# Kernel tuning notes

Measured on AMD Instinct MI355X. Metric: run time of the kernel, lower is better.

## Reference

```python
import jax, jax.numpy as jnp
import numpy as np
import math

B, S, E, H = 4, 1024, 1024, 16
D = E // H
C = 1.0           # Poincare ball curvature
CS = math.sqrt(C)
EPS = 1e-7

def _sq(x):
    return jnp.sum(x * x, axis=-1, keepdims=True)

def expmap0(v):
    n = jnp.sqrt(jnp.clip(_sq(v), 1e-15))
    return jnp.tanh(CS * n) * v / (CS * n)

def logmap0(y):
    n = jnp.sqrt(jnp.clip(_sq(y), 1e-15))
    t = jnp.clip(CS * n, 0.0, 1.0 - 1e-6)
    return jnp.arctanh(t) * y / (CS * n)

def hlinear(x, z, r):
    # Poincare fully-connected layer (HNN++, Shimizu et al.), as in hypll HLinear
    lam = 2.0 / jnp.clip(1.0 - C * _sq(x), EPS)          # [..., 1] conformal factor
    zn = jnp.clip(jnp.linalg.norm(z, axis=0), 1e-15)     # [out]
    xz = x @ z                                           # [..., out]
    tcr = 2.0 * CS * r
    v = (2.0 * zn / CS) * jnp.arcsinh(CS * lam * xz / zn * jnp.cosh(tcr) - (lam - 1.0) * jnp.sinh(tcr))
    w = jnp.sinh(CS * v) / CS
    return w / (1.0 + jnp.sqrt(1.0 + C * jnp.sum(w * w, -1, keepdims=True)))

def _beta(a, b):
    return math.exp(math.lgamma(a) + math.lgamma(b) - math.lgamma(a + b))

def _forward(query, key, value, zq, bq, zk, bk, zv, bv):
    pq, pk, pv = hlinear(query, zq, bq), hlinear(key, zk, bk), hlinear(value, zv, bv)
    split = lambda x: x.reshape(B, S, H, D).transpose(0, 2, 1, 3)   # [B,H,S,D]
    q, k, v = split(pq), split(pk), split(pv)
    # attention_similarity: negative per-head pairwise Poincare distance (all heads vectorized)
    q2 = jnp.sum(q * q, -1)                              # [B,H,Sq]
    k2 = jnp.sum(k * k, -1)                              # [B,H,Sk]
    qk = jnp.einsum('bhqd,bhkd->bhqk', q, k)
    diff2 = jnp.clip(q2[..., :, None] + k2[..., None, :] - 2.0 * qk, 0.0)
    den = jnp.clip((1.0 - C * q2)[..., :, None] * (1.0 - C * k2)[..., None, :], EPS)
    dist = jnp.arccosh(jnp.clip(1.0 + 2.0 * C * diff2 / den, 1.0 + 1e-6)) / CS
    # attention_activation: softmax over keys
    w = jax.nn.softmax(-dist, axis=-1)                   # [B,H,Sq,Sk]
    # attention_midpoint: weighted gyromidpoint of values over keys
    lam = 2.0 / jnp.clip(1.0 - C * jnp.sum(v * v, -1), EPS)          # [B,H,Sk]
    num = jnp.einsum('bhqk,bhkd->bhqd', w * lam[..., None, :], v)
    dnm = jnp.clip(jnp.einsum('bhqk,bhk->bhq', jnp.abs(w), lam - 1.0), EPS)
    u = num / dnm[..., None]
    mid = u / (1.0 + jnp.sqrt(jnp.clip(1.0 - C * _sq(u), EPS)))      # (1/2) Mobius scalar mult
    # manifold.cat: beta-concatenation of heads (HNN++)
    scale = _beta(E / 2.0, 0.5) / _beta(D / 2.0, 0.5)
    tv = logmap0(mid) * scale                            # tangent at origin, [B,H,S,D]
    return expmap0(tv.transpose(0, 2, 1, 3).reshape(B, S, E))

def setup_inputs():
    key = jax.random.key(0)
    ks = jax.random.split(key, 9)
    mk = lambda k: expmap0(jax.random.normal(k, (B, S, E), jnp.float32) * (0.3 / math.sqrt(E)))
    zs = lambda k: jax.random.normal(k, (E, E), jnp.float32) / math.sqrt(E)
    bs = lambda k: jax.random.normal(k, (E,), jnp.float32) * 0.01
    return {"query": mk(ks[0]), "key": mk(ks[1]), "value": mk(ks[2]),
            "zq": zs(ks[3]), "bq": bs(ks[4]), "zk": zs(ks[5]), "bk": bs(ks[6]),
            "zv": zs(ks[7]), "bv": bs(ks[8])}

def reference(query, key, value, zq, bq, zk, bk, zv, bv):
    return _forward(query, key, value, zq, bq, zk, bk, zv, bv)
```

## Files before the change

kernel.cpp:

```cpp
#include <hip/hip_runtime.h>
#include <cmath>

#define EPSF 1e-7f

constexpr int B_ = 4, S_ = 1024, E_ = 1024, H_ = 16, D_ = 64;
constexpr int BS_ = B_ * S_;

typedef __attribute__((ext_vector_type(8))) short bf16x8;
typedef __attribute__((ext_vector_type(4))) float f32x4;

__device__ inline unsigned int fbits(float f) { union { float f; unsigned int u; } x; x.f = f; return x.u; }
__device__ inline float ubits(unsigned int u) { union { unsigned int u; float f; } x; x.u = u; return x.f; }

__device__ inline unsigned short f2bf(float f) {
  unsigned int u = fbits(f);
  unsigned int r = u + 0x7fffu + ((u >> 16) & 1u);
  return (unsigned short)(r >> 16);
}
__device__ inline float bf2f(unsigned short h) { return ubits(((unsigned int)h) << 16); }
__device__ inline float fastrcp(float x) { return __builtin_amdgcn_rcpf(x); }

__device__ __forceinline__ void async_ld16(const unsigned short* g, unsigned short* l) {
  __builtin_amdgcn_global_load_lds(
      (const __attribute__((address_space(1))) unsigned int*)g,
      (__attribute__((address_space(3))) unsigned int*)l, 16, 0, 0);
}

__device__ __forceinline__ unsigned int cvt_pk_bf16(float lo, float hi) {
  unsigned int r;
  asm("v_cvt_pk_bf16_f32 %0, %1, %2" : "=v"(r) : "v"(lo), "v"(hi));
  return r;
}
__device__ __forceinline__ void permlane32_swap(unsigned int &a, unsigned int &b) {
  asm("v_permlane32_swap_b32 %0, %1" : "+v"(a), "+v"(b));
}
__device__ __forceinline__ void permlane16_swap(unsigned int &a, unsigned int &b) {
  asm("v_permlane16_swap_b32 %0, %1" : "+v"(a), "+v"(b));
}

__global__ __launch_bounds__(256) void xsplit_kernel(
    const float* __restrict__ xq, const float* __restrict__ xk,
    const float* __restrict__ xv, unsigned short* __restrict__ Xbf,
    float* __restrict__ lamRow) {
  const int row = blockIdx.x;
  const float* x = (row < BS_) ? xq : (row < 2 * BS_ ? xk : xv);
  const int r = row & (BS_ - 1);
  const int tid = threadIdx.x;
  float4 v = ((const float4*)(x + (size_t)r * E_))[tid];
  float s = v.x * v.x + v.y * v.y + v.z * v.z + v.w * v.w;
  #pragma unroll
  for (int m = 1; m < 64; m <<= 1) s += __shfl_xor(s, m, 64);
  __shared__ float red[4];
  if ((tid & 63) == 0) red[tid >> 6] = s;
  __syncthreads();
  s = red[0] + red[1] + red[2] + red[3];
  uint2 p;
  p.x = (unsigned int)f2bf(v.x) | ((unsigned int)f2bf(v.y) << 16);
  p.y = (unsigned int)f2bf(v.z) | ((unsigned int)f2bf(v.w) << 16);
  ((uint2*)(Xbf + (size_t)row * E_))[tid] = p;
  if (tid == 0) lamRow[row] = 2.0f / fmaxf(1.0f - s, EPSF);
}

__global__ __launch_bounds__(256) void zsplit_kernel(
    const float* __restrict__ zq, const float* __restrict__ zk, const float* __restrict__ zv,
    unsigned short* __restrict__ BhiT, float* __restrict__ Zpart) {
  const int mat = blockIdx.z;
  const float* z = mat == 0 ? zq : (mat == 1 ? zk : zv);
  const int k0 = blockIdx.y * 64, n0 = blockIdx.x * 64;
  __shared__ float t[64][65];
  __shared__ float sred[64][4];
  const int tid = threadIdx.x;
  {
    int kr = tid >> 4, nc = (tid & 15) * 4;
    #pragma unroll
    for (int i = 0; i < 4; i++) {
      float4 vv = *(const float4*)(z + (size_t)(k0 + kr + i * 16) * E_ + n0 + nc);
      t[kr + i * 16][nc + 0] = vv.x;
      t[kr + i * 16][nc + 1] = vv.y;
      t[kr + i * 16][nc + 2] = vv.z;
      t[kr + i * 16][nc + 3] = vv.w;
    }
  }
  __syncthreads();
  int nr = tid >> 2, kc = (tid & 3) * 16;
  unsigned int ph[8];
  float ss = 0.f;
  #pragma unroll
  for (int p = 0; p < 8; p++) {
    float x0 = t[kc + 2 * p][nr], x1 = t[kc + 2 * p + 1][nr];
    ph[p] = (unsigned int)f2bf(x0) | ((unsigned int)f2bf(x1) << 16);
    ss += x0 * x0 + x1 * x1;
  }
  size_t off = (size_t)mat * E_ * E_ + (size_t)(n0 + nr) * E_ + k0 + kc;
  uint4* dh = (uint4*)(BhiT + off);
  dh[0] = make_uint4(ph[0], ph[1], ph[2], ph[3]);
  dh[1] = make_uint4(ph[4], ph[5], ph[6], ph[7]);
  sred[nr][tid & 3] = ss;
  __syncthreads();
  if (tid < 64) {
    float v = sred[tid][0] + sred[tid][1] + sred[tid][2] + sred[tid][3];
    Zpart[(size_t)(mat * 16 + blockIdx.y) * E_ + n0 + tid] = v;
  }
}

__global__ __launch_bounds__(256) void zstat_final_kernel(
    const float* __restrict__ Zpart,
    const float* __restrict__ bq, const float* __restrict__ bk, const float* __restrict__ bv,
    float* __restrict__ znA, float* __restrict__ chA, float* __restrict__ shA) {
  const int idx = blockIdx.x * 256 + threadIdx.x;
  const int mat = idx >> 10, col = idx & 1023;
  const float* bb = mat == 0 ? bq : (mat == 1 ? bk : bv);
  float s = 0.f;
  #pragma unroll
  for (int ky = 0; ky < 16; ky++)
    s += Zpart[(size_t)(mat * 16 + ky) * E_ + col];
  float n = fmaxf(sqrtf(s), 1e-15f);
  znA[idx] = n;
  float rb = bb[col];
  chA[idx] = coshf(2.f * rb);
  shA[idx] = sinhf(2.f * rb);
}

__global__ __launch_bounds__(256, 3) void hlinear_mfma_kernel(
    const unsigned short* __restrict__ Xbf,
    const unsigned short* __restrict__ BhiT,
    const float* __restrict__ lamRow, const float* __restrict__ znA,
    const float* __restrict__ chA, const float* __restrict__ shA,
    unsigned short* __restrict__ Wbf) {
  const int mat = blockIdx.z;
  const unsigned short* xa = Xbf + (size_t)mat * BS_ * E_;
  const unsigned short* bh = BhiT + (size_t)mat * E_ * E_;
  const int lid = blockIdx.y * 8 + blockIdx.x;
  const int sqi = lid >> 4, offb = lid & 15;
  const int m0 = ((sqi >> 1) * 4 + (offb & 3)) * 128;
  const int n0 = ((sqi & 1) * 4 + (offb >> 2)) * 128;

  __shared__ unsigned short LDSU[18432];
  unsigned short* As = LDSU;
  unsigned short* Bh = LDSU + 8192;

  const int tid = threadIdx.x;
  const int wid = tid >> 6, lane = tid & 63, quad = lane >> 4, l16 = lane & 15;
  const int wm = (wid >> 1) * 64, wn = (wid & 1) * 64;

  f32x4 acc[4][4];
  #pragma unroll
  for (int i = 0; i < 4; i++)
    #pragma unroll
    for (int j = 0; j < 4; j++) acc[i][j] = (f32x4){0.f, 0.f, 0.f, 0.f};

  const int lrow = lane >> 3;
  const int lcs = ((lane & 7) ^ lrow) * 8;
  const int xsw = (l16 & 7);

  for (int kt = 0; kt < E_ / 64; ++kt) {
    __syncthreads();
    const int kb = kt * 64 + lcs;
    #pragma unroll
    for (int c2 = 0; c2 < 4; c2++) {
      const int c = wid * 4 + c2;
      const int grow = c * 8 + lrow;
      async_ld16(xa + (size_t)(m0 + grow) * E_ + kb, As + c * 512);
      async_ld16(bh + (size_t)(n0 + grow) * E_ + kb, Bh + c * 512);
    }
    __syncthreads();
    #pragma unroll
    for (int h = 0; h < 2; h++) {
      bf16x8 a[4];
      #pragma unroll
      for (int mt = 0; mt < 4; mt++) {
        int row = wm + mt * 16 + l16;
        a[mt] = *(const bf16x8*)&As[row * 64 + (((h * 4 + quad) ^ xsw) * 8)];
      }
      #pragma unroll
      for (int nt = 0; nt < 4; nt++) {
        int row = wn + nt * 16 + l16;
        bf16x8 bhf = *(const bf16x8*)&Bh[row * 64 + (((h * 4 + quad) ^ xsw) * 8)];
        #pragma unroll
        for (int mt = 0; mt < 4; mt++)
          acc[mt][nt] = __builtin_amdgcn_mfma_f32_16x16x32_bf16(a[mt], bhf, acc[mt][nt], 0, 0, 0);
      }
    }
  }

  const float* lamP = lamRow + mat * BS_;
  float lamv[16];
  #pragma unroll
  for (int mt = 0; mt < 4; mt++)
    #pragma unroll
    for (int r = 0; r < 4; r++)
      lamv[mt * 4 + r] = lamP[m0 + wm + mt * 16 + quad * 4 + r];

  __syncthreads();
  unsigned short* epi = LDSU + wid * 4608;
  #pragma unroll
  for (int nt = 0; nt < 4; nt++) {
    int cg = n0 + wn + nt * 16 + l16;
    float zn = znA[mat * E_ + cg];
    float chzn = chA[mat * E_ + cg] / zn;
    float sh = shA[mat * E_ + cg];
    float tzn = 2.f * zn;
    #pragma unroll
    for (int mt = 0; mt < 4; mt++) {
      #pragma unroll
      for (int r = 0; r < 4; r++) {
        float lam = lamv[mt * 4 + r];
        float arg = fmaf(lam * acc[mt][nt][r], chzn, -(lam - 1.f) * sh);
        float sq2 = sqrtf(fmaf(arg, arg, 1.f));
        float v = tzn * __logf(arg + sq2);
        float ev = __expf(v);
        float w = 0.5f * (ev - fastrcp(ev));
        epi[(mt * 16 + quad * 4 + r) * 72 + nt * 16 + l16] = f2bf(w);
      }
    }
  }
  unsigned short* gout = Wbf + (size_t)mat * BS_ * E_ + (size_t)(m0 + wm) * E_ + n0 + wn;
  const int rrow = lane >> 3, seg = lane & 7;
  #pragma unroll
  for (int i = 0; i < 8; i++) {
    int row = i * 8 + rrow;
    uint4 val = *(const uint4*)&epi[row * 72 + seg * 8];
    *(uint4*)(gout + (size_t)row * E_ + seg * 8) = val;
  }
}

__global__ __launch_bounds__(256) void normalize_kernel(
    const unsigned short* __restrict__ Wbf, unsigned short* __restrict__ Pbf,
    float* __restrict__ HN) {
  const unsigned short* w = Wbf + (size_t)blockIdx.x * E_;
  int tid = threadIdx.x;
  uint2 wv = ((const uint2*)w)[tid];
  float w0 = bf2f((unsigned short)(wv.x & 0xFFFF));
  float w1 = bf2f((unsigned short)(wv.x >> 16));
  float w2 = bf2f((unsigned short)(wv.y & 0xFFFF));
  float w3 = bf2f((unsigned short)(wv.y >> 16));
  float s = w0 * w0 + w1 * w1 + w2 * w2 + w3 * w3;
  #pragma unroll
  for (int m = 1; m < 64; m <<= 1) s += __shfl_xor(s, m, 64);
  __shared__ float red[4];
  if ((tid & 63) == 0) red[tid >> 6] = s;
  __syncthreads();
  s = red[0] + red[1] + red[2] + red[3];
  float t = 1.f / (1.f + sqrtf(1.f + s));
  unsigned short p0 = f2bf(w0 * t), p1 = f2bf(w1 * t), p2 = f2bf(w2 * t), p3 = f2bf(w3 * t);
  uint2 pk;
  pk.x = (unsigned int)p0 | ((unsigned int)p1 << 16);
  pk.y = (unsigned int)p2 | ((unsigned int)p3 << 16);
  ((uint2*)(Pbf + (size_t)blockIdx.x * E_))[tid] = pk;
  float r0 = bf2f(p0), r1 = bf2f(p1), r2 = bf2f(p2), r3 = bf2f(p3);
  float hs = r0 * r0 + r1 * r1 + r2 * r2 + r3 * r3;
  hs += __shfl_xor(hs, 1, 64);
  hs += __shfl_xor(hs, 2, 64);
  hs += __shfl_xor(hs, 4, 64);
  hs += __shfl_xor(hs, 8, 64);
  if ((tid & 15) == 0) HN[(size_t)blockIdx.x * H_ + (tid >> 4)] = hs;
}

__global__ __launch_bounds__(256) void vtrans_kernel(
    const unsigned short* __restrict__ Pbf, const float* __restrict__ HN,
    unsigned short* __restrict__ KsG, unsigned short* __restrict__ VtG,
    unsigned short* __restrict__ lamMG, unsigned int* __restrict__ auxG) {
  const int st = blockIdx.x, h = blockIdx.y, b = blockIdx.z;
  const unsigned short* pk = Pbf + (size_t)BS_ * E_;
  const unsigned short* pv = Pbf + (size_t)2 * BS_ * E_;
  const float* hnk = HN + (size_t)BS_ * H_;
  const float* hnv = HN + (size_t)2 * BS_ * H_;
  __shared__ unsigned short T[64][72];
  __shared__ float lamS[64], cS[64];
  const int tid = threadIdx.x;
  const size_t bhS = (size_t)(b * H_ + h) * S_;
  {
    int lr = tid >> 2, lc = (tid & 3) * 16;
    const uint4* src = (const uint4*)(pv + (size_t)(b * S_ + st * 64 + lr) * E_ + h * 64 + lc);
    *(uint4*)&T[lr][lc] = src[0];
    *(uint4*)&T[lr][lc + 8] = src[1];
  }
  if (tid < 64) {
    float v2 = hnv[(size_t)(b * S_ + st * 64 + tid) * H_ + h];
    float lam = 2.f / fmaxf(1.f - v2, EPSF);
    lamS[tid] = lam;
    size_t sidx = bhS + st * 64 + tid;
    lamMG[sidx] = f2bf(lam - 1.f);
    float k2 = hnk[(size_t)(b * S_ + st * 64 + tid) * H_ + h];
    float rc = fastrcp(1.f - k2);
    cS[tid] = rc;
    auxG[sidx] = (unsigned int)f2bf(rc) | ((unsigned int)f2bf(rc * k2) << 16);
  }
  __syncthreads();
  {
    int d = tid >> 2, sc = (tid & 3) * 16;
    unsigned int o[8];
    #pragma unroll
    for (int i = 0; i < 8; i++) {
      int s0 = sc + 2 * i;
      float f0 = bf2f(T[s0][d]) * lamS[s0];
      float f1 = bf2f(T[s0 + 1][d]) * lamS[s0 + 1];
      o[i] = (unsigned int)f2bf(f0) | ((unsigned int)f2bf(f1) << 16);
    }
    unsigned short* dst = VtG + (bhS * 64) + (size_t)d * S_ + st * 64 + sc;
    ((uint4*)dst)[0] = make_uint4(o[0], o[1], o[2], o[3]);
    ((uint4*)dst)[1] = make_uint4(o[4], o[5], o[6], o[7]);
  }
  {
    int lr = tid >> 2, lc = (tid & 3) * 16;
    float c = cS[lr];
    const uint4* src = (const uint4*)(pk + (size_t)(b * S_ + st * 64 + lr) * E_ + h * 64 + lc);
    union { uint4 q; unsigned short s[8]; } i0, i1, o0, o1;
    i0.q = src[0]; i1.q = src[1];
    #pragma unroll
    for (int j = 0; j < 8; j++) {
      o0.s[j] = f2bf(bf2f(i0.s[j]) * c);
      o1.s[j] = f2bf(bf2f(i1.s[j]) * c);
    }
    unsigned short* dst = KsG + (bhS + st * 64 + lr) * 64 + lc;
    ((uint4*)dst)[0] = o0.q;
    ((uint4*)dst)[1] = o1.q;
  }
}

__global__ __launch_bounds__(512) void attention_kernel(
    const unsigned short* __restrict__ Pbf, const float* __restrict__ HN,
    const unsigned short* __restrict__ KsG, const unsigned short* __restrict__ VtG,
    const unsigned short* __restrict__ lamMG, const unsigned int* __restrict__ auxG,
    float* __restrict__ TV, float scale) {
  const int qt = blockIdx.x, h = blockIdx.y, b = blockIdx.z;
  const unsigned short* pq = Pbf;
  const float* hnq = HN;

  const int tid = threadIdx.x;
  const int wid = tid >> 6, lane = tid & 63;
  const int quad = lane >> 4, l16 = lane & 15;

  __shared__ __align__(16) unsigned short Kl[2][4096];
  __shared__ __align__(16) unsigned short Vl[2][4096];
  __shared__ __align__(16) unsigned short lamL[1024];
  __shared__ __align__(16) unsigned int auxL[1024];

  const size_t bhS = (size_t)(b * H_ + h) * S_;
  ((unsigned int*)lamL)[tid] = ((const unsigned int*)(lamMG + bhS))[tid];
  ((uint2*)auxL)[tid] = ((const uint2*)(auxG + bhS))[tid];

  const int qrow0 = qt * 128 + wid * 16;
  const size_t qgrow = ((size_t)(b * S_ + qrow0 + l16)) * E_ + h * 64;
  bf16x8 aq0r = *(const bf16x8*)(pq + qgrow + quad * 8);
  bf16x8 aq1r = *(const bf16x8*)(pq + qgrow + 32 + quad * 8);
  const float q2l = hnq[((size_t)(b * S_ + qrow0 + l16)) * H_ + h];
  const float al = 2.f * fastrcp(1.f - q2l);
  const float sc2 = -2.f * al;
  bf16x8 aq0, aq1;
  #pragma unroll
  for (int j = 0; j < 8; j++) {
    aq0[j] = (short)f2bf(bf2f((unsigned short)aq0r[j]) * sc2);
    aq1[j] = (short)f2bf(bf2f((unsigned short)aq1r[j]) * sc2);
  }
  const unsigned short ae0 = (quad == 0) ? f2bf(al * q2l) : 0;
  const unsigned short ae1 = (quad == 0) ? f2bf(al) : 0;
  const bf16x8 aex = (bf16x8){(short)ae0, (short)ae1, 0, 0, 0, 0, 0, 0};

  f32x4 accO[4];
  #pragma unroll
  for (int dt = 0; dt < 4; dt++) accO[dt] = (f32x4){0.f, 0.f, 0.f, 0.f};
  f32x4 accD = (f32x4){0.f, 0.f, 0.f, 0.f};

  const int lr = lane >> 3, cch = lane & 7;
  const int xsw = l16 & 7;
  const unsigned short* kbase = KsG + bhS * 64;
  const unsigned short* vbase = VtG + bhS * 64;
  const int srow = wid * 8 + lr;
  const int scc = ((cch ^ lr) * 8);

  async_ld16(kbase + (size_t)srow * 64 + scc, &Kl[0][wid * 512]);
  async_ld16(vbase + (size_t)srow * S_ + scc, &Vl[0][wid * 512]);
  __syncthreads();

  for (int kt = 0; kt < S_ / 64; ++kt) {
    const int buf = kt & 1;
    if (kt + 1 < S_ / 64) {
      async_ld16(kbase + (size_t)((kt + 1) * 64 + srow) * 64 + scc, &Kl[buf ^ 1][wid * 512]);
      async_ld16(vbase + (size_t)srow * S_ + (kt + 1) * 64 + scc, &Vl[buf ^ 1][wid * 512]);
    }

    unsigned int Wp[4][2];
    #pragma unroll
    for (int nt = 0; nt < 4; nt++) {
      const int krow = nt * 16 + l16;
      bf16x8 bk0 = *(const bf16x8*)&Kl[buf][krow * 64 + ((quad ^ xsw) * 8)];
      bf16x8 bk1 = *(const bf16x8*)&Kl[buf][krow * 64 + (((4 + quad) ^ xsw) * 8)];
      unsigned int av = (quad == 0) ? auxL[kt * 64 + krow] : 0u;
      bf16x8 bex = (bf16x8){(short)(av & 0xFFFF), (short)(av >> 16), 0, 0, 0, 0, 0, 0};
      f32x4 z = (f32x4){0.f, 0.f, 0.f, 0.f};
      f32x4 st = __builtin_amdgcn_mfma_f32_16x16x32_bf16(bex, aex, z, 0, 0, 0);
      st = __builtin_amdgcn_mfma_f32_16x16x32_bf16(bk0, aq0, st, 0, 0, 0);
      st = __builtin_amdgcn_mfma_f32_16x16x32_bf16(bk1, aq1, st, 0, 0, 0);
      float w[4];
      #pragma unroll
      for (int r2 = 0; r2 < 4; r2++) {
        float t = fmaxf(st[r2], 1e-6f);
        float A = 1.f + t;
        w[r2] = A - sqrtf(fmaf(A, A, -1.f));
      }
      Wp[nt][0] = cvt_pk_bf16(w[0], w[1]);
      Wp[nt][1] = cvt_pk_bf16(w[2], w[3]);
    }
    unsigned int x00 = Wp[0][0], y00 = Wp[1][0];
    permlane32_swap(x00, y00); permlane16_swap(x00, y00);
    unsigned int x01 = Wp[0][1], y01 = Wp[1][1];
    permlane32_swap(x01, y01); permlane16_swap(x01, y01);
    unsigned int x10 = Wp[2][0], y10 = Wp[3][0];
    permlane32_swap(x10, y10); permlane16_swap(x10, y10);
    unsigned int x11 = Wp[2][1], y11 = Wp[3][1];
    permlane32_swap(x11, y11); permlane16_swap(x11, y11);
    union { unsigned int u[4]; bf16x8 v; } ap0u, ap1u;
    ap0u.u[0] = x00; ap0u.u[1] = x01; ap0u.u[2] = y00; ap0u.u[3] = y01;
    ap1u.u[0] = x10; ap1u.u[1] = x11; ap1u.u[2] = y10; ap1u.u[3] = y11;
    const bf16x8 ap0 = ap0u.v, ap1 = ap1u.v;

    #pragma unroll
    for (int dt = 0; dt < 4; dt++) {
      const int drow = dt * 16 + l16;
      bf16x8 bv0 = *(const bf16x8*)&Vl[buf][drow * 64 + ((quad ^ xsw) * 8)];
      bf16x8 bv1 = *(const bf16x8*)&Vl[buf][drow * 64 + (((4 + quad) ^ xsw) * 8)];
      accO[dt] = __builtin_amdgcn_mfma_f32_16x16x32_bf16(ap0, bv0, accO[dt], 0, 0, 0);
      accO[dt] = __builtin_amdgcn_mfma_f32_16x16x32_bf16(ap1, bv1, accO[dt], 0, 0, 0);
    }
    bf16x8 bl0 = *(const bf16x8*)&lamL[kt * 64 + quad * 8];
    bf16x8 bl1 = *(const bf16x8*)&lamL[kt * 64 + 32 + quad * 8];
    accD = __builtin_amdgcn_mfma_f32_16x16x32_bf16(ap0, bl0, accD, 0, 0, 0);
    accD = __builtin_amdgcn_mfma_f32_16x16x32_bf16(ap1, bl1, accD, 0, 0, 0);

    __syncthreads();
  }

  #pragma unroll
  for (int r2 = 0; r2 < 4; r2++) {
    float rdsum = 1.f / accD[r2];
    float uu[4];
    float su = 0.f;
    #pragma unroll
    for (int dt = 0; dt < 4; dt++) { uu[dt] = accO[dt][r2] * rdsum; su += uu[dt] * uu[dt]; }
    su += __shfl_xor(su, 1, 64);
    su += __shfl_xor(su, 2, 64);
    su += __shfl_xor(su, 4, 64);
    su += __shfl_xor(su, 8, 64);
    float g = 1.f / (1.f + sqrtf(fmaxf(1.f - su, EPSF)));
    float n2 = fmaxf(su * g * g, 1e-15f);
    float n = sqrtf(n2);
    float fac = atanhf(fminf(n, 1.f - 1e-6f)) / n * g * scale;
    size_t orow = ((size_t)(b * S_ + qrow0 + quad * 4 + r2)) * E_ + h * 64 + l16;
    #pragma unroll
    for (int dt = 0; dt < 4; dt++) TV[orow + dt * 16] = fac * uu[dt];
  }
}

__global__ __launch_bounds__(256) void expmap_kernel(float* __restrict__ TV) {
  float* w = TV + (size_t)blockIdx.x * E_;
  int tid = threadIdx.x;
  float4 v = ((float4*)w)[tid];
  float s = v.x * v.x + v.y * v.y + v.z * v.z + v.w * v.w;
  #pragma unroll
  for (int m = 1; m < 64; m <<= 1) s += __shfl_xor(s, m, 64);
  __shared__ float red[4];
  if ((tid & 63) == 0) red[tid >> 6] = s;
  __syncthreads();
  s = red[0] + red[1] + red[2] + red[3];
  float n = sqrtf(fmaxf(s, 1e-15f));
  float f = tanhf(n) / n;
  v.x *= f; v.y *= f; v.z *= f; v.w *= f;
  ((float4*)w)[tid] = v;
}

extern "C" void kernel_launch(void* const* d_in, const int* in_sizes, int n_in,
                              void* d_out, int out_size, void* d_ws, size_t ws_size,
                              hipStream_t stream) {
  (void)in_sizes; (void)n_in; (void)out_size; (void)ws_size;
  const float* q  = (const float*)d_in[0];
  const float* k  = (const float*)d_in[1];
  const float* v  = (const float*)d_in[2];
  const float* zq = (const float*)d_in[3];
  const float* bq = (const float*)d_in[4];
  const float* zk = (const float*)d_in[5];
  const float* bk = (const float*)d_in[6];
  const float* zv = (const float*)d_in[7];
  const float* bv = (const float*)d_in[8];

  unsigned short* Wbf = (unsigned short*)d_ws;
  unsigned short* Pbf = Wbf + (size_t)3 * BS_ * E_;
  unsigned short* BhiT = Pbf;
  unsigned short* Xbf = Pbf + (size_t)3 * BS_ * E_;
  float* HN           = (float*)(Xbf + (size_t)3 * BS_ * E_);
  float* lamRow       = HN + (size_t)3 * BS_ * H_;
  float* znA          = lamRow + 3 * BS_;
  float* chA          = znA + 3 * E_;
  float* shA          = chA + 3 * E_;
  float* Zpart        = shA + 3 * E_;
  unsigned short* VtG = (unsigned short*)(Zpart + 48 * E_);
  unsigned short* KsG = VtG + (size_t)B_ * H_ * 64 * S_;
  unsigned short* lamMG = KsG + (size_t)B_ * H_ * S_ * 64;
  unsigned int* auxG  = (unsigned int*)(lamMG + (size_t)B_ * H_ * S_);
  float* out          = (float*)d_out;

  double lb1 = lgamma(E_ / 2.0) + lgamma(0.5) - lgamma(E_ / 2.0 + 0.5);
  double lb2 = lgamma(D_ / 2.0) + lgamma(0.5) - lgamma(D_ / 2.0 + 0.5);
  float scale = (float)exp(lb1 - lb2);

  hipLaunchKernelGGL(xsplit_kernel, dim3(3 * BS_), dim3(256), 0, stream, q, k, v, Xbf, lamRow);
  hipLaunchKernelGGL(zsplit_kernel, dim3(16, 16, 3), dim3(256), 0, stream,
                     zq, zk, zv, BhiT, Zpart);
  hipLaunchKernelGGL(zstat_final_kernel, dim3(12), dim3(256), 0, stream,
                     Zpart, bq, bk, bv, znA, chA, shA);
  hipLaunchKernelGGL(hlinear_mfma_kernel, dim3(8, 32, 3), dim3(256), 0, stream,
                     Xbf, BhiT, lamRow, znA, chA, shA, Wbf);
  hipLaunchKernelGGL(normalize_kernel, dim3(3 * BS_), dim3(256), 0, stream, Wbf, Pbf, HN);
  hipLaunchKernelGGL(vtrans_kernel, dim3(16, 16, 4), dim3(256), 0, stream,
                     Pbf, HN, KsG, VtG, lamMG, auxG);
  hipLaunchKernelGGL(attention_kernel, dim3(8, 16, 4), dim3(512), 0, stream,
                     Pbf, HN, KsG, VtG, lamMG, auxG, out, scale);
  hipLaunchKernelGGL(expmap_kernel, dim3(BS_), dim3(256), 0, stream, out);
}
```

Before: 252.4 us.

## Triple-buffer attention K/V loads, remap blocks to XCDs, use fast sqrt/rcp

Moves the attention kernel's K/V tiles from double to triple buffering. Prefetches run two tiles ahead, and the full __syncthreads is replaced by a partial vmcnt wait plus a raw barrier, so loads overlap more compute. It also flattens the grid to 1D and remaps block IDs so that all query tiles of one (batch, head) land on the same XCD, improving L2 reuse of K/V. Precise sqrt and divides are swapped for hardware approximations, which costs a little accuracy. LDS use per block grows by a third, which may lower occupancy.

```diff
diff --git a/kernel.cpp b/kernel.cpp
--- a/kernel.cpp
+++ b/kernel.cpp
@@ -19,6 +19,7 @@
 }
 __device__ inline float bf2f(unsigned short h) { return ubits(((unsigned int)h) << 16); }
 __device__ inline float fastrcp(float x) { return __builtin_amdgcn_rcpf(x); }
+__device__ inline float fastsqrt(float x) { return __builtin_amdgcn_sqrtf(x); }
 
 __device__ __forceinline__ void async_ld16(const unsigned short* g, unsigned short* l) {
   __builtin_amdgcn_global_load_lds(
@@ -323,7 +324,12 @@
     const unsigned short* __restrict__ KsG, const unsigned short* __restrict__ VtG,
     const unsigned short* __restrict__ lamMG, const unsigned int* __restrict__ auxG,
     float* __restrict__ TV, float scale) {
-  const int qt = blockIdx.x, h = blockIdx.y, b = blockIdx.z;
+  const int fid = blockIdx.x;
+  const int xcd = fid & 7, slot = fid >> 3;
+  const int group = xcd + 8 * (slot >> 3);
+  const int qt = slot & 7;
+  const int h = group & 15, b = group >> 4;
+
   const unsigned short* pq = Pbf;
   const float* hnq = HN;
 
@@ -331,12 +337,24 @@
   const int wid = tid >> 6, lane = tid & 63;
   const int quad = lane >> 4, l16 = lane & 15;
 
-  __shared__ __align__(16) unsigned short Kl[2][4096];
-  __shared__ __align__(16) unsigned short Vl[2][4096];
+  __shared__ __align__(16) unsigned short Kl[3][4096];
+  __shared__ __align__(16) unsigned short Vl[3][4096];
   __shared__ __align__(16) unsigned short lamL[1024];
   __shared__ __align__(16) unsigned int auxL[1024];
 
   const size_t bhS = (size_t)(b * H_ + h) * S_;
+  const int lr = lane >> 3, cch = lane & 7;
+  const int xsw = l16 & 7;
+  const unsigned short* kbase = KsG + bhS * 64;
+  const unsigned short* vbase = VtG + bhS * 64;
+  const int srow = wid * 8 + lr;
+  const int scc = ((cch ^ lr) * 8);
+
+  async_ld16(kbase + (size_t)srow * 64 + scc, &Kl[0][wid * 512]);
+  async_ld16(vbase + (size_t)srow * S_ + scc, &Vl[0][wid * 512]);
+  async_ld16(kbase + (size_t)(64 + srow) * 64 + scc, &Kl[1][wid * 512]);
+  async_ld16(vbase + (size_t)(srow * S_ + 64) + scc, &Vl[1][wid * 512]);
+
   ((unsigned int*)lamL)[tid] = ((const unsigned int*)(lamMG + bhS))[tid];
   ((uint2*)auxL)[tid] = ((const uint2*)(auxG + bhS))[tid];
 
@@ -362,30 +380,26 @@
   for (int dt = 0; dt < 4; dt++) accO[dt] = (f32x4){0.f, 0.f, 0.f, 0.f};
   f32x4 accD = (f32x4){0.f, 0.f, 0.f, 0.f};
 
-  const int lr = lane >> 3, cch = lane & 7;
-  const int xsw = l16 & 7;
-  const unsigned short* kbase = KsG + bhS * 64;
-  const unsigned short* vbase = VtG + bhS * 64;
-  const int srow = wid * 8 + lr;
-  const int scc = ((cch ^ lr) * 8);
-
-  async_ld16(kbase + (size_t)srow * 64 + scc, &Kl[0][wid * 512]);
-  async_ld16(vbase + (size_t)srow * S_ + scc, &Vl[0][wid * 512]);
-  __syncthreads();
-
-  for (int kt = 0; kt < S_ / 64; ++kt) {
-    const int buf = kt & 1;
-    if (kt + 1 < S_ / 64) {
-      async_ld16(kbase + (size_t)((kt + 1) * 64 + srow) * 64 + scc, &Kl[buf ^ 1][wid * 512]);
-      async_ld16(vbase + (size_t)srow * S_ + (kt + 1) * 64 + scc, &Vl[buf ^ 1][wid * 512]);
-    }
+  asm volatile("s_waitcnt vmcnt(0) lgkmcnt(0)" ::: "memory");
+  __builtin_amdgcn_s_barrier();
+
+  const int NT = S_ / 64;
+  int cur = 0, pf = 2;
+  #pragma unroll 1
+  for (int kt = 0; kt < NT; ++kt) {
+    if (kt + 2 < NT) {
+      async_ld16(kbase + (size_t)((kt + 2) * 64 + srow) * 64 + scc, &Kl[pf][wid * 512]);
+      async_ld16(vbase + (size_t)(srow * S_ + (kt + 2) * 64) + scc, &Vl[pf][wid * 512]);
+    }
+    const unsigned short* Kb = Kl[cur];
+    const unsigned short* Vb = Vl[cur];
 
     unsigned int Wp[4][2];
     #pragma unroll
     for (int nt = 0; nt < 4; nt++) {
       const int krow = nt * 16 + l16;
-      bf16x8 bk0 = *(const bf16x8*)&Kl[buf][krow * 64 + ((quad ^ xsw) * 8)];
-      bf16x8 bk1 = *(const bf16x8*)&Kl[buf][krow * 64 + (((4 + quad) ^ xsw) * 8)];
+      bf16x8 bk0 = *(const bf16x8*)&Kb[krow * 64 + ((quad ^ xsw) * 8)];
+      bf16x8 bk1 = *(const bf16x8*)&Kb[krow * 64 + (((4 + quad) ^ xsw) * 8)];
       unsigned int av = (quad == 0) ? auxL[kt * 64 + krow] : 0u;
       bf16x8 bex = (bf16x8){(short)(av & 0xFFFF), (short)(av >> 16), 0, 0, 0, 0, 0, 0};
       f32x4 z = (f32x4){0.f, 0.f, 0.f, 0.f};
@@ -397,7 +411,7 @@
       for (int r2 = 0; r2 < 4; r2++) {
         float t = fmaxf(st[r2], 1e-6f);
         float A = 1.f + t;
-        w[r2] = A - sqrtf(fmaf(A, A, -1.f));
+        w[r2] = A - fastsqrt(fmaf(A, A, -1.f));
       }
       Wp[nt][0] = cvt_pk_bf16(w[0], w[1]);
       Wp[nt][1] = cvt_pk_bf16(w[2], w[3]);
@@ -418,8 +432,8 @@
     #pragma unroll
     for (int dt = 0; dt < 4; dt++) {
       const int drow = dt * 16 + l16;
-      bf16x8 bv0 = *(const bf16x8*)&Vl[buf][drow * 64 + ((quad ^ xsw) * 8)];
-      bf16x8 bv1 = *(const bf16x8*)&Vl[buf][drow * 64 + (((4 + quad) ^ xsw) * 8)];
+      bf16x8 bv0 = *(const bf16x8*)&Vb[drow * 64 + ((quad ^ xsw) * 8)];
+      bf16x8 bv1 = *(const bf16x8*)&Vb[drow * 64 + (((4 + quad) ^ xsw) * 8)];
       accO[dt] = __builtin_amdgcn_mfma_f32_16x16x32_bf16(ap0, bv0, accO[dt], 0, 0, 0);
       accO[dt] = __builtin_amdgcn_mfma_f32_16x16x32_bf16(ap1, bv1, accO[dt], 0, 0, 0);
     }
@@ -428,12 +442,19 @@
     accD = __builtin_amdgcn_mfma_f32_16x16x32_bf16(ap0, bl0, accD, 0, 0, 0);
     accD = __builtin_amdgcn_mfma_f32_16x16x32_bf16(ap1, bl1, accD, 0, 0, 0);
 
-    __syncthreads();
+    if (kt + 2 < NT) {
+      asm volatile("s_waitcnt vmcnt(2)" ::: "memory");
+    } else {
+      asm volatile("s_waitcnt vmcnt(0)" ::: "memory");
+    }
+    __builtin_amdgcn_s_barrier();
+    cur = (cur == 2) ? 0 : cur + 1;
+    pf = (pf == 2) ? 0 : pf + 1;
   }
 
   #pragma unroll
   for (int r2 = 0; r2 < 4; r2++) {
-    float rdsum = 1.f / accD[r2];
+    float rdsum = fastrcp(accD[r2]);
     float uu[4];
     float su = 0.f;
     #pragma unroll
@@ -442,10 +463,10 @@
     su += __shfl_xor(su, 2, 64);
     su += __shfl_xor(su, 4, 64);
     su += __shfl_xor(su, 8, 64);
-    float g = 1.f / (1.f + sqrtf(fmaxf(1.f - su, EPSF)));
+    float g = fastrcp(1.f + fastsqrt(fmaxf(1.f - su, EPSF)));
     float n2 = fmaxf(su * g * g, 1e-15f);
-    float n = sqrtf(n2);
-    float fac = atanhf(fminf(n, 1.f - 1e-6f)) / n * g * scale;
+    float n = fastsqrt(n2);
+    float fac = atanhf(fminf(n, 1.f - 1e-6f)) * fastrcp(n) * g * scale;
     size_t orow = ((size_t)(b * S_ + qrow0 + quad * 4 + r2)) * E_ + h * 64 + l16;
     #pragma unroll
     for (int dt = 0; dt < 4; dt++) TV[orow + dt * 16] = fac * uu[dt];
@@ -513,7 +534,7 @@
   hipLaunchKernelGGL(normalize_kernel, dim3(3 * BS_), dim3(256), 0, stream, Wbf, Pbf, HN);
   hipLaunchKernelGGL(vtrans_kernel, dim3(16, 16, 4), dim3(256), 0, stream,
                      Pbf, HN, KsG, VtG, lamMG, auxG);
-  hipLaunchKernelGGL(attention_kernel, dim3(8, 16, 4), dim3(512), 0, stream,
+  hipLaunchKernelGGL(attention_kernel, dim3(512), dim3(512), 0, stream,
                      Pbf, HN, KsG, VtG, lamMG, auxG, out, scale);
   hipLaunchKernelGGL(expmap_kernel, dim3(BS_), dim3(256), 0, stream, out);
 }
```

New measurement: 216.6 us. -14.2%, faster.
